# Kernel optimization log

Hardware: AMD Instinct MI355X
Metric: run time of the kernel (lower is better)

Reference implementation:

```python
import jax, jax.numpy as jnp
import numpy as np

W_WIN = 5        # fine_window_size
D_F = 128        # fine d_model
D_C = 256        # coarse d_model
B, HF, WF = 2, 208, 208
WC = 104
LC = WC * WC
N = 5000


def setup_inputs() -> dict:
    key = jax.random.key(0)
    ks = jax.random.split(key, 12)
    inp = {
        'feat_f0': jax.random.normal(ks[0], (B, D_F, HF, WF), jnp.float32),
        'feat_f1': jax.random.normal(ks[1], (B, D_F, HF, WF), jnp.float32),
        'feat_c0': jax.random.normal(ks[2], (B, LC, D_C), jnp.float32),
        'feat_c1': jax.random.normal(ks[3], (B, LC, D_C), jnp.float32),
        # linear layer params (stored as [in, out]; torch weight is [out, in])
        'corr_fuse_w': jax.random.normal(ks[4], (3 * D_F, D_F), jnp.float32) * 0.05,
        'corr_fuse_b': jnp.zeros((D_F,), jnp.float32),
        'down_proj_w': jax.random.normal(ks[5], (D_C, D_F), jnp.float32) * 0.05,
        'down_proj_b': jnp.zeros((D_F,), jnp.float32),
        'merge_feat_w': jax.random.normal(ks[6], (2 * D_F, D_F), jnp.float32) * 0.05,
        'merge_feat_b': jnp.zeros((D_F,), jnp.float32),
        'b_ids': jax.random.randint(ks[7], (N,), 0, B),
        'i_ids': jax.random.randint(ks[8], (N,), 0, LC),
        'j_ids': jax.random.randint(ks[9], (N,), 0, LC),
        'w0c': WC,
        'w1c': WC,
    }
    return inp


def _extract_patches(feat, b_ids, x_ids, y_ids, W):
    # Equivalent to F.unfold(feat, W, stride=1, padding=W//2) followed by a
    # gather at linear index y*width+x: directly gather the WxW window
    # centered at (x, y) with zero padding. feat: [B, C, H, Wd].
    Bsz, C, H, Wd = feat.shape
    off = jnp.arange(W) - W // 2
    yy = (y_ids[:, None] + off)[:, :, None]          # [n, W, 1]
    xx = (x_ids[:, None] + off)[:, None, :]          # [n, 1, W]
    valid = (yy >= 0) & (yy < H) & (xx >= 0) & (xx < Wd)  # [n, W, W]
    yc = jnp.clip(yy, 0, H - 1)
    xc = jnp.clip(xx, 0, Wd - 1)
    # advanced-index gather -> [n, W, W, C] (kernel rows outer, cols inner,
    # channel last: matches unfold's C-major layout after view/transpose)
    p = feat[b_ids[:, None, None], :, yc, xc]
    p = p * valid[..., None].astype(feat.dtype)
    return p.reshape(p.shape[0], W * W, C)           # [n, ww, C]


def reference(feat_f0, feat_f1, feat_c0, feat_c1,
              corr_fuse_w, corr_fuse_b, down_proj_w, down_proj_b,
              merge_feat_w, merge_feat_b,
              b_ids, i_ids, j_ids, w0c, w1c):
    W = W_WIN
    ww = W * W
    d_f = feat_f0.shape[1]
    Hf0, Wf0 = feat_f0.shape[2], feat_f0.shape[3]
    Hf1, Wf1 = feat_f1.shape[2], feat_f1.shape[3]

    x0 = jnp.clip((i_ids % w0c) * 2, 0, Wf0 - 1)
    y0 = jnp.clip((i_ids // w0c) * 2, 0, Hf0 - 1)
    x1 = jnp.clip((j_ids % w1c) * 2, 0, Wf1 - 1)
    y1 = jnp.clip((j_ids // w1c) * 2, 0, Hf1 - 1)

    p0 = _extract_patches(feat_f0, b_ids, x0, y0, W)   # [N, ww, d_f]
    p1 = _extract_patches(feat_f1, b_ids, x1, y1, W)

    inv_s = 1.0 / (d_f ** 0.5)
    c_patch = p0 * p1 * inv_s
    ctx_map = feat_f1.mean(axis=(2, 3))[b_ids][:, None, :]   # [N, 1, d_f]
    c_uav = p0 * ctx_map * inv_s
    ctx_uav = feat_f0.mean(axis=(2, 3))[b_ids][:, None, :]
    c_map = p1 * ctx_uav * inv_s

    f0 = jnp.concatenate([c_patch, c_uav, c_map], -1) @ corr_fuse_w + corr_fuse_b
    f1 = jnp.concatenate([c_patch, c_map, c_uav], -1) @ corr_fuse_w + corr_fuse_b

    # cat_c_feat branch
    fc = jnp.concatenate([feat_c0[b_ids, i_ids], feat_c1[b_ids, j_ids]], 0)
    fc = fc @ down_proj_w + down_proj_b                       # [2N, d_f]
    fc_rep = jnp.broadcast_to(fc[:, None, :], (fc.shape[0], ww, fc.shape[1]))
    merged = jnp.concatenate([jnp.concatenate([f0, f1], 0), fc_rep], -1)
    merged = merged @ merge_feat_w + merge_feat_b             # [2N, ww, d_f]

    n = f0.shape[0]
    return merged[:n], merged[n:]
```

## Files before the change

kernel.cpp:

```cpp
#include <hip/hip_runtime.h>

#define HF   208
#define WF   208
#define D_C  256
#define LC   10816
#define NPTS 5000
#define HW   (HF*WF)
#define INV_S 0.08838834764831845f
#define PAD  136

typedef __bf16 bf16_t;
typedef __bf16 bf16x8 __attribute__((ext_vector_type(8)));
typedef float  f32x4  __attribute__((ext_vector_type(4)));

#define FTR_OFF   172032
#define FTR_BYTES ((size_t)2*2*HW*128*2)
#define G_OFF     (FTR_OFF + FTR_BYTES)
#define G_BYTES   ((size_t)2*NPTS*128*4)

__global__ __launch_bounds__(256) void ptg_kernel(
    const float* __restrict__ f0, const float* __restrict__ f1,
    const float* __restrict__ fc0, const float* __restrict__ fc1,
    const float* __restrict__ corr_w, const float* __restrict__ corr_b,
    const float* __restrict__ dp_w,   const float* __restrict__ dp_b,
    const float* __restrict__ mg_w,   const float* __restrict__ mg_b,
    const int* __restrict__ b_ids, const int* __restrict__ i_ids,
    const int* __restrict__ j_ids,
    bf16_t* __restrict__ A_swz, bf16_t* __restrict__ DmB,
    float* __restrict__ bias_all,
    bf16_t* __restrict__ ftr, float* __restrict__ ctxs,
    float* __restrict__ g) {
  __shared__ union {
    struct { float tile[64][129]; float cred[128]; } tr;
    float s_src[16][256];
  } sm;
  int bid = blockIdx.x;
  int tid = threadIdx.x;

  if (bid < 641) {
    if (tid >= 128) return;
    int c = tid;
    if (bid < 384) {
      int mat = bid >> 7, r = bid & 127;
      float acc = 0.f;
      for (int t = 0; t < 128; ++t)
        acc += corr_w[(mat * 128 + r) * 128 + t] * mg_w[t * 128 + c];
      if (mat == 0) acc *= INV_S;
      int ks = r >> 5, quad = (r & 31) >> 3, jj = r & 7;
      int nt = c >> 4, lr = c & 15;
      A_swz[mat * 16384 + (((nt * 4 + ks) * 64) + quad * 16 + lr) * 8 + jj] = (bf16_t)acc;
    } else if (bid < 640) {
      int r = bid - 384;
      float acc = 0.f;
      for (int t = 0; t < 128; ++t)
        acc += dp_w[r * 128 + t] * mg_w[(128 + t) * 128 + c];
      DmB[(((r >> 3) * 128) + c) * 8 + (r & 7)] = (bf16_t)acc;
    } else {
      float acc = mg_b[c];
      for (int t = 0; t < 128; ++t) {
        acc += corr_b[t] * mg_w[t * 128 + c];
        acc += dp_b[t]   * mg_w[(128 + t) * 128 + c];
      }
      bias_all[c] = acc;
    }
    return;
  }

  if (bid >= 3345) {
    int r0 = (bid - 3345) * 16;
    for (int u = tid; u < 16 * 256; u += 256) {
      int rr = u >> 8, t = u & 255;
      int r = r0 + rr;
      const float* src;
      int b, idx;
      if (r < NPTS) { b = b_ids[r]; idx = i_ids[r]; src = fc0; }
      else          { b = b_ids[r - NPTS]; idx = j_ids[r - NPTS]; src = fc1; }
      sm.s_src[rr][t] = src[((size_t)b * LC + idx) * D_C + t];
    }
    __syncthreads();
    int col = tid & 127, half = tid >> 7;
    float h[8];
    {
      float db = dp_b[col];
#pragma unroll
      for (int r8 = 0; r8 < 8; ++r8) h[r8] = db;
      for (int t = 0; t < 256; t += 4) {
        f32x4 wv;
#pragma unroll
        for (int k = 0; k < 4; ++k) wv[k] = dp_w[(t + k) * 128 + col];
#pragma unroll
        for (int r8 = 0; r8 < 8; ++r8) {
          f32x4 sv = *(const f32x4*)&sm.s_src[half * 8 + r8][t];
          h[r8] += sv[0] * wv[0] + sv[1] * wv[1] + sv[2] * wv[2] + sv[3] * wv[3];
        }
      }
    }
    __syncthreads();
    float* s_h = &sm.s_src[0][0];
#pragma unroll
    for (int r8 = 0; r8 < 8; ++r8) s_h[(half * 8 + r8) * 128 + col] = h[r8];
    __syncthreads();
    float acc2[8];
    float mb = mg_b[col];
#pragma unroll
    for (int r8 = 0; r8 < 8; ++r8) acc2[r8] = mb;
    for (int t = 0; t < 128; t += 4) {
      f32x4 wv;
#pragma unroll
      for (int k = 0; k < 4; ++k) wv[k] = mg_w[(128 + t + k) * 128 + col];
#pragma unroll
      for (int r8 = 0; r8 < 8; ++r8) {
        f32x4 sv = *(const f32x4*)&s_h[(half * 8 + r8) * 128 + t];
        acc2[r8] += sv[0] * wv[0] + sv[1] * wv[1] + sv[2] * wv[2] + sv[3] * wv[3];
      }
    }
    float cp = 0.f;
    for (int t = 0; t < 128; ++t) cp += corr_b[t] * mg_w[t * 128 + col];
#pragma unroll
    for (int r8 = 0; r8 < 8; ++r8)
      g[(size_t)(r0 + half * 8 + r8) * 128 + col] = acc2[r8] + cp;
    return;
  }

  bid -= 641;
  int tb = bid / 676;
  int hw0 = (bid % 676) * 64;
  const float* src = (tb < 2 ? f0 : f1) + (size_t)((tb & 1) * 128) * HW;
  if (tid < 128) sm.tr.cred[tid] = 0.f;
  int w4 = (tid & 15) * 4, cr = tid >> 4;
  for (int c = cr; c < 128; c += 16) {
    f32x4 v = *(const f32x4*)&src[(size_t)c * HW + hw0 + w4];
#pragma unroll
    for (int j = 0; j < 4; ++j) sm.tr.tile[w4 + j][c] = v[j];
  }
  __syncthreads();
  bf16_t* dst = ftr + ((size_t)tb * HW + hw0) * 128;
  int cb = (tid & 15) * 8;
  float sums8[8] = {0, 0, 0, 0, 0, 0, 0, 0};
  for (int p = (tid >> 4); p < 64; p += 16) {
    bf16x8 v;
#pragma unroll
    for (int j = 0; j < 8; ++j) {
      float x = sm.tr.tile[p][cb + j];
      sums8[j] += x;
      v[j] = (bf16_t)x;
    }
    *(bf16x8*)(dst + (size_t)p * 128 + cb) = v;
  }
  int lane = tid & 63;
#pragma unroll
  for (int j = 0; j < 8; ++j) {
    float s = sums8[j];
    s += __shfl_down(s, 32, 64);
    s += __shfl_down(s, 16, 64);
    if (lane < 16) atomicAdd(&sm.tr.cred[cb + j], s);
  }
  __syncthreads();
  if (tid < 128) atomicAdd(&ctxs[tb * 128 + tid], sm.tr.cred[tid]);
}

__global__ __launch_bounds__(256, 6) void main_kernel(
    const bf16_t* __restrict__ ftr,
    const int* __restrict__ b_ids, const int* __restrict__ i_ids,
    const int* __restrict__ j_ids, const int* __restrict__ w0c_p,
    const int* __restrict__ w1c_p, const float* __restrict__ ctxs,
    const bf16_t* __restrict__ A_swz, const float* __restrict__ g,
    float* __restrict__ out) {
  __shared__ __align__(16) union {
    bf16_t sV[3][32][PAD];
    float  so[2][25 * 128];
  } sm;

  int n = blockIdx.x;
  int tid = threadIdx.x;
  int b = b_ids[n], ii = i_ids[n], jj = j_ids[n];
  int w0c = w0c_p[0], w1c = w1c_p[0];
  int x0 = min((ii % w0c) * 2, WF - 1), y0 = min((ii / w0c) * 2, HF - 1);
  int x1 = min((jj % w1c) * 2, WF - 1), y1 = min((jj / w1c) * 2, HF - 1);

  int grp = tid >> 3, e = tid & 7;
  if (grp < 25) {
    const bf16_t* base0 = ftr + (size_t)b * HW * 128;
    const bf16_t* base1 = ftr + (size_t)(2 + b) * HW * 128;
    int dy = grp / 5 - 2, dx = grp % 5 - 2;
    int ya = y0 + dy, xa = x0 + dx;
    int yb = y1 + dy, xb = x1 + dx;
    bool v0 = (ya >= 0 && ya < HF && xa >= 0 && xa < WF);
    bool v1 = (yb >= 0 && yb < HF && xb >= 0 && xb < WF);
    const bf16_t* r0 = base0 + ((size_t)(v0 ? ya * WF + xa : 0)) * 128;
    const bf16_t* r1 = base1 + ((size_t)(v1 ? yb * WF + xb : 0)) * 128;
    const float ksc = INV_S / (float)HW;
#pragma unroll
    for (int h = 0; h < 2; ++h) {
      int cb = h * 64 + e * 8;
      bf16x8 a0 = *(const bf16x8*)(r0 + cb);
      bf16x8 a1 = *(const bf16x8*)(r1 + cb);
      f32x4 cs0a = *(const f32x4*)&ctxs[b * 128 + cb];
      f32x4 cs0b = *(const f32x4*)&ctxs[b * 128 + cb + 4];
      f32x4 cs1a = *(const f32x4*)&ctxs[256 + b * 128 + cb];
      f32x4 cs1b = *(const f32x4*)&ctxs[256 + b * 128 + cb + 4];
      bf16x8 oP, o1, o2;
#pragma unroll
      for (int j = 0; j < 8; ++j) {
        float p0 = v0 ? (float)a0[j] : 0.f;
        float p1 = v1 ? (float)a1[j] : 0.f;
        float c0f = (j < 4 ? cs0a[j & 3] : cs0b[j & 3]) * ksc;
        float c1f = (j < 4 ? cs1a[j & 3] : cs1b[j & 3]) * ksc;
        oP[j] = (bf16_t)(p0 * p1);
        o1[j] = (bf16_t)(p0 * c1f);
        o2[j] = (bf16_t)(p1 * c0f);
      }
      *(bf16x8*)&sm.sV[0][grp][cb] = oP;
      *(bf16x8*)&sm.sV[1][grp][cb] = o1;
      *(bf16x8*)&sm.sV[2][grp][cb] = o2;
    }
  }
  __syncthreads();

  int w = tid >> 6, lane = tid & 63, quad = lane >> 4, lr = lane & 15;
  f32x4 accP[2][2] = {};
  f32x4 acc01[2][2] = {};
  f32x4 acc10[2][2] = {};

#pragma unroll
  for (int ks = 0; ks < 4; ++ks) {
    bf16x8 va[2][3];
#pragma unroll
    for (int mt = 0; mt < 2; ++mt)
#pragma unroll
      for (int m = 0; m < 3; ++m)
        va[mt][m] = *(const bf16x8*)&sm.sV[m][mt * 16 + lr][ks * 32 + quad * 8];
    bf16x8 vb[3][2];
#pragma unroll
    for (int m = 0; m < 3; ++m)
#pragma unroll
      for (int ntl = 0; ntl < 2; ++ntl) {
        int nt = w * 2 + ntl;
        vb[m][ntl] = *(const bf16x8*)(A_swz + m * 16384 + (((nt * 4 + ks) * 64) + lane) * 8);
      }
#pragma unroll
    for (int mt = 0; mt < 2; ++mt)
#pragma unroll
      for (int ntl = 0; ntl < 2; ++ntl) {
        accP[mt][ntl]  = __builtin_amdgcn_mfma_f32_16x16x32_bf16(va[mt][0], vb[0][ntl], accP[mt][ntl], 0, 0, 0);
        acc01[mt][ntl] = __builtin_amdgcn_mfma_f32_16x16x32_bf16(va[mt][1], vb[1][ntl], acc01[mt][ntl], 0, 0, 0);
        acc01[mt][ntl] = __builtin_amdgcn_mfma_f32_16x16x32_bf16(va[mt][2], vb[2][ntl], acc01[mt][ntl], 0, 0, 0);
        acc10[mt][ntl] = __builtin_amdgcn_mfma_f32_16x16x32_bf16(va[mt][2], vb[1][ntl], acc10[mt][ntl], 0, 0, 0);
        acc10[mt][ntl] = __builtin_amdgcn_mfma_f32_16x16x32_bf16(va[mt][1], vb[2][ntl], acc10[mt][ntl], 0, 0, 0);
      }
  }
  __syncthreads();

#pragma unroll
  for (int ntl = 0; ntl < 2; ++ntl) {
    int col = w * 32 + ntl * 16 + lr;
#pragma unroll
    for (int mt = 0; mt < 2; ++mt)
#pragma unroll
      for (int rg = 0; rg < 4; ++rg) {
        int row = mt * 16 + quad * 4 + rg;
        if (row < 25) {
          sm.so[0][row * 128 + col] = accP[mt][ntl][rg] + acc01[mt][ntl][rg];
          sm.so[1][row * 128 + col] = accP[mt][ntl][rg] + acc10[mt][ntl][rg];
        }
      }
  }
  __syncthreads();

  float* o0 = out + (size_t)n * 3200;
  float* o1 = out + (size_t)NPTS * 3200 + (size_t)n * 3200;
  const float* g0 = g + (size_t)n * 128;
  const float* g1 = g + (size_t)(NPTS + n) * 128;
  for (int i = tid; i < 800; i += 256) {
    int f = i * 4, c = f & 127;
    f32x4 gv0 = *(const f32x4*)(g0 + c);
    f32x4 gv1 = *(const f32x4*)(g1 + c);
    f32x4 v0 = *(const f32x4*)&sm.so[0][f];
    f32x4 v1 = *(const f32x4*)&sm.so[1][f];
    __builtin_nontemporal_store(v0 + gv0, (f32x4*)(o0 + f));
    __builtin_nontemporal_store(v1 + gv1, (f32x4*)(o1 + f));
  }
}

__global__ __launch_bounds__(256) void ctx_mean_f32_kernel(
    const float* __restrict__ f0, const float* __restrict__ f1,
    float* __restrict__ ctxs) {
  int id = blockIdx.x;
  const float* src = (id < 256 ? f0 : f1) + (size_t)(id & 255) * HW;
  float s = 0.f;
  for (int i = threadIdx.x; i < HW; i += 256) s += src[i];
  for (int off = 32; off > 0; off >>= 1) s += __shfl_down(s, off, 64);
  __shared__ float part[4];
  if ((threadIdx.x & 63) == 0) part[threadIdx.x >> 6] = s;
  __syncthreads();
  if (threadIdx.x == 0) ctxs[id] = part[0] + part[1] + part[2] + part[3];
}

__global__ __launch_bounds__(256, 4) void main_fallback_kernel(
    const float* __restrict__ f0, const float* __restrict__ f1,
    const float* __restrict__ fc0, const float* __restrict__ fc1,
    const int* __restrict__ b_ids, const int* __restrict__ i_ids,
    const int* __restrict__ j_ids, const int* __restrict__ w0c_p,
    const int* __restrict__ w1c_p, const float* __restrict__ ctxs,
    const float* __restrict__ bias_all, const bf16_t* __restrict__ A_swz,
    const bf16_t* __restrict__ DmB, float* __restrict__ out) {
  __shared__ __align__(16) bf16_t sV[3][32][PAD];
  __shared__ float sg[2][128];
  int n = blockIdx.x;
  int tid = threadIdx.x;
  int b = b_ids[n], ii = i_ids[n], jj = j_ids[n];
  int w0c = w0c_p[0], w1c = w1c_p[0];
  int x0 = min((ii % w0c) * 2, WF - 1), y0 = min((ii / w0c) * 2, HF - 1);
  int x1 = min((jj % w1c) * 2, WF - 1), y1 = min((jj / w1c) * 2, HF - 1);
  const float ksc = INV_S / (float)HW;
  int c = tid & 127, kh = tid >> 7;
  float cs0 = ctxs[b * 128 + c] * ksc;
  float cs1 = ctxs[256 + b * 128 + c] * ksc;
  const float* f0b = f0 + (size_t)(b * 128 + c) * HW;
  const float* f1b = f1 + (size_t)(b * 128 + c) * HW;
  for (int k = kh; k < 32; k += 2) {
    float p0 = 0.f, p1 = 0.f;
    if (k < 25) {
      int dy = k / 5 - 2, dx = k % 5 - 2;
      int ya = y0 + dy, xa = x0 + dx;
      if (ya >= 0 && ya < HF && xa >= 0 && xa < WF) p0 = f0b[ya * WF + xa];
      int yb = y1 + dy, xb = x1 + dx;
      if (yb >= 0 && yb < HF && xb >= 0 && xb < WF) p1 = f1b[yb * WF + xb];
    }
    sV[0][k][c] = (bf16_t)(p0 * p1);
    sV[1][k][c] = (bf16_t)(p0 * cs1);
    sV[2][k][c] = (bf16_t)(p1 * cs0);
  }
  {
    int h = tid >> 7, col = tid & 127;
    const float* fcrow = h ? fc1 + ((size_t)b * LC + jj) * D_C
                           : fc0 + ((size_t)b * LC + ii) * D_C;
    const bf16_t* dbase = DmB + col * 8;
    float p0 = 0.f, p1 = 0.f, p2 = 0.f, p3 = 0.f;
#pragma unroll 4
    for (int t8 = 0; t8 < 32; ++t8) {
      bf16x8 d  = *(const bf16x8*)(dbase + t8 * 1024);
      f32x4  fa = *(const f32x4*)(fcrow + t8 * 8);
      f32x4  fb = *(const f32x4*)(fcrow + t8 * 8 + 4);
      p0 += fa[0] * (float)d[0] + fb[0] * (float)d[4];
      p1 += fa[1] * (float)d[1] + fb[1] * (float)d[5];
      p2 += fa[2] * (float)d[2] + fb[2] * (float)d[6];
      p3 += fa[3] * (float)d[3] + fb[3] * (float)d[7];
    }
    sg[h][col] = ((p0 + p1) + (p2 + p3));
  }
  __syncthreads();
  int w = tid >> 6, lane = tid & 63, quad = lane >> 4, lr = lane & 15;
  f32x4 accP[2][2] = {}, acc01[2][2] = {}, acc10[2][2] = {};
#pragma unroll
  for (int ks = 0; ks < 4; ++ks) {
    bf16x8 va[2][3];
#pragma unroll
    for (int mt = 0; mt < 2; ++mt)
#pragma unroll
      for (int m = 0; m < 3; ++m)
        va[mt][m] = *(const bf16x8*)&sV[m][mt * 16 + lr][ks * 32 + quad * 8];
    bf16x8 vb[3][2];
#pragma unroll
    for (int m = 0; m < 3; ++m)
#pragma unroll
      for (int ntl = 0; ntl < 2; ++ntl) {
        int nt = w * 2 + ntl;
        vb[m][ntl] = *(const bf16x8*)(A_swz + m * 16384 + (((nt * 4 + ks) * 64) + lane) * 8);
      }
#pragma unroll
    for (int mt = 0; mt < 2; ++mt)
#pragma unroll
      for (int ntl = 0; ntl < 2; ++ntl) {
        accP[mt][ntl]  = __builtin_amdgcn_mfma_f32_16x16x32_bf16(va[mt][0], vb[0][ntl], accP[mt][ntl], 0, 0, 0);
        acc01[mt][ntl] = __builtin_amdgcn_mfma_f32_16x16x32_bf16(va[mt][1], vb[1][ntl], acc01[mt][ntl], 0, 0, 0);
        acc01[mt][ntl] = __builtin_amdgcn_mfma_f32_16x16x32_bf16(va[mt][2], vb[2][ntl], acc01[mt][ntl], 0, 0, 0);
        acc10[mt][ntl] = __builtin_amdgcn_mfma_f32_16x16x32_bf16(va[mt][2], vb[1][ntl], acc10[mt][ntl], 0, 0, 0);
        acc10[mt][ntl] = __builtin_amdgcn_mfma_f32_16x16x32_bf16(va[mt][1], vb[2][ntl], acc10[mt][ntl], 0, 0, 0);
      }
  }
#pragma unroll
  for (int ntl = 0; ntl < 2; ++ntl) {
    int col = w * 32 + ntl * 16 + lr;
    float bg = bias_all[col];
    float gg0 = sg[0][col] + bg, gg1 = sg[1][col] + bg;
#pragma unroll
    for (int mt = 0; mt < 2; ++mt)
#pragma unroll
      for (int rg = 0; rg < 4; ++rg) {
        int row = mt * 16 + quad * 4 + rg;
        if (row < 25) {
          size_t o = ((size_t)n * 25 + row) * 128 + col;
          out[o] = accP[mt][ntl][rg] + acc01[mt][ntl][rg] + gg0;
          out[(size_t)NPTS * 25 * 128 + o] = accP[mt][ntl][rg] + acc10[mt][ntl][rg] + gg1;
        }
      }
  }
}

extern "C" void kernel_launch(void* const* d_in, const int* in_sizes, int n_in,
                              void* d_out, int out_size, void* d_ws, size_t ws_size,
                              hipStream_t stream) {
  const float* f0     = (const float*)d_in[0];
  const float* f1     = (const float*)d_in[1];
  const float* fc0    = (const float*)d_in[2];
  const float* fc1    = (const float*)d_in[3];
  const float* corr_w = (const float*)d_in[4];
  const float* corr_b = (const float*)d_in[5];
  const float* dp_w   = (const float*)d_in[6];
  const float* dp_b   = (const float*)d_in[7];
  const float* mg_w   = (const float*)d_in[8];
  const float* mg_b   = (const float*)d_in[9];
  const int* b_ids    = (const int*)d_in[10];
  const int* i_ids    = (const int*)d_in[11];
  const int* j_ids    = (const int*)d_in[12];
  const int* w0c      = (const int*)d_in[13];
  const int* w1c      = (const int*)d_in[14];

  char* ws = (char*)d_ws;
  float*  ctxs     = (float*)(ws);
  float*  bias_all = (float*)(ws + 4096);
  bf16_t* A_swz    = (bf16_t*)(ws + 8192);
  bf16_t* DmB      = (bf16_t*)(ws + 106496);
  bf16_t* ftr      = (bf16_t*)(ws + FTR_OFF);
  float*  g        = (float*)(ws + G_OFF);
  int fast = (ws_size >= G_OFF + G_BYTES) ? 1 : 0;

  if (fast) {
    hipMemsetAsync(ctxs, 0, 2048, stream);
    ptg_kernel<<<3970, 256, 0, stream>>>(
        f0, f1, fc0, fc1, corr_w, corr_b, dp_w, dp_b, mg_w, mg_b,
        b_ids, i_ids, j_ids, A_swz, DmB, bias_all, ftr, ctxs, g);
    main_kernel<<<NPTS, 256, 0, stream>>>(ftr, b_ids, i_ids, j_ids, w0c, w1c,
                                          ctxs, A_swz, g, (float*)d_out);
  } else {
    ptg_kernel<<<641, 256, 0, stream>>>(
        f0, f1, fc0, fc1, corr_w, corr_b, dp_w, dp_b, mg_w, mg_b,
        b_ids, i_ids, j_ids, A_swz, DmB, bias_all, ftr, ctxs, g);
    ctx_mean_f32_kernel<<<512, 256, 0, stream>>>(f0, f1, ctxs);
    main_fallback_kernel<<<NPTS, 256, 0, stream>>>(f0, f1, fc0, fc1, b_ids,
                                                   i_ids, j_ids, w0c, w1c, ctxs,
                                                   bias_all, A_swz, DmB,
                                                   (float*)d_out);
  }
}
```

Before: 347.7 us.

## Store transpose tile as bf16, reduce channel sums in registers, reorder block roles

The transpose part of the prep kernel now converts to bf16 when writing the shared-memory tile, which halves LDS use. It computes per-channel sums with 16-lane shuffles straight from the loaded vectors, so the second pass over shared memory and the shared atomics go away, and it writes rows with vector bf16x8 reads. The g-projection blocks are moved to the front of the grid and the launch bounds ask for 8 blocks per CU, so the heavier work starts early and occupancy rises. The fallback path has to detect its smaller grid by checking gridDim, which adds coupling between the two paths.

```diff
diff --git a/kernel.cpp b/kernel.cpp
--- a/kernel.cpp
+++ b/kernel.cpp
@@ -9,6 +9,11 @@
 #define INV_S 0.08838834764831845f
 #define PAD  136
 
+#define G_BLOCKS    625
+#define PREP_BLOCKS 641
+#define TR_BLOCKS   2704
+#define PTG_GRID    (G_BLOCKS + PREP_BLOCKS + TR_BLOCKS)
+
 typedef __bf16 bf16_t;
 typedef __bf16 bf16x8 __attribute__((ext_vector_type(8)));
 typedef float  f32x4  __attribute__((ext_vector_type(4)));
@@ -18,7 +23,7 @@
 #define G_OFF     (FTR_OFF + FTR_BYTES)
 #define G_BYTES   ((size_t)2*NPTS*128*4)
 
-__global__ __launch_bounds__(256) void ptg_kernel(
+__global__ __launch_bounds__(256, 8) void ptg_kernel(
     const float* __restrict__ f0, const float* __restrict__ f1,
     const float* __restrict__ fc0, const float* __restrict__ fc1,
     const float* __restrict__ corr_w, const float* __restrict__ corr_b,
@@ -30,18 +35,25 @@
     float* __restrict__ bias_all,
     bf16_t* __restrict__ ftr, float* __restrict__ ctxs,
     float* __restrict__ g) {
-  __shared__ union {
-    struct { float tile[64][129]; float cred[128]; } tr;
+  __shared__ __align__(16) union {
+    struct { bf16_t tile[64][136]; float cred[128]; } tr;
     float s_src[16][256];
   } sm;
   int bid = blockIdx.x;
   int tid = threadIdx.x;
 
-  if (bid < 641) {
+  int prep_id = -1;
+  if (gridDim.x == 641) {
+    prep_id = bid;
+  } else if (bid >= G_BLOCKS && bid < G_BLOCKS + PREP_BLOCKS) {
+    prep_id = bid - G_BLOCKS;
+  }
+
+  if (prep_id >= 0) {
     if (tid >= 128) return;
     int c = tid;
-    if (bid < 384) {
-      int mat = bid >> 7, r = bid & 127;
+    if (prep_id < 384) {
+      int mat = prep_id >> 7, r = prep_id & 127;
       float acc = 0.f;
       for (int t = 0; t < 128; ++t)
         acc += corr_w[(mat * 128 + r) * 128 + t] * mg_w[t * 128 + c];
@@ -49,8 +61,8 @@
       int ks = r >> 5, quad = (r & 31) >> 3, jj = r & 7;
       int nt = c >> 4, lr = c & 15;
       A_swz[mat * 16384 + (((nt * 4 + ks) * 64) + quad * 16 + lr) * 8 + jj] = (bf16_t)acc;
-    } else if (bid < 640) {
-      int r = bid - 384;
+    } else if (prep_id < 640) {
+      int r = prep_id - 384;
       float acc = 0.f;
       for (int t = 0; t < 128; ++t)
         acc += dp_w[r * 128 + t] * mg_w[(128 + t) * 128 + c];
@@ -66,8 +78,8 @@
     return;
   }
 
-  if (bid >= 3345) {
-    int r0 = (bid - 3345) * 16;
+  if (bid < G_BLOCKS) {
+    int r0 = bid * 16;
     for (int u = tid; u < 16 * 256; u += 256) {
       int rr = u >> 8, t = u & 255;
       int r = r0 + rr;
@@ -122,41 +134,40 @@
     return;
   }
 
-  bid -= 641;
-  int tb = bid / 676;
-  int hw0 = (bid % 676) * 64;
+  int tbid = bid - (G_BLOCKS + PREP_BLOCKS);
+  int tb = tbid / 676;
+  int hw0 = (tbid % 676) * 64;
   const float* src = (tb < 2 ? f0 : f1) + (size_t)((tb & 1) * 128) * HW;
-  if (tid < 128) sm.tr.cred[tid] = 0.f;
-  int w4 = (tid & 15) * 4, cr = tid >> 4;
-  for (int c = cr; c < 128; c += 16) {
+  int wg = tid & 15, cr = tid >> 4;
+  int w4 = wg * 4;
+  float csum[8];
+#pragma unroll
+  for (int k = 0; k < 8; ++k) {
+    int c = cr + k * 16;
     f32x4 v = *(const f32x4*)&src[(size_t)c * HW + hw0 + w4];
-#pragma unroll
-    for (int j = 0; j < 4; ++j) sm.tr.tile[w4 + j][c] = v[j];
-  }
-  __syncthreads();
+    csum[k] = (v[0] + v[1]) + (v[2] + v[3]);
+#pragma unroll
+    for (int j = 0; j < 4; ++j) sm.tr.tile[w4 + j][c] = (bf16_t)v[j];
+  }
+#pragma unroll
+  for (int k = 0; k < 8; ++k) {
+    float s = csum[k];
+    s += __shfl_down(s, 8, 16);
+    s += __shfl_down(s, 4, 16);
+    s += __shfl_down(s, 2, 16);
+    s += __shfl_down(s, 1, 16);
+    if (wg == 0) sm.tr.cred[cr + k * 16] = s;
+  }
+  __syncthreads();
+  if (tid < 128) atomicAdd(&ctxs[tb * 128 + tid], sm.tr.cred[tid]);
   bf16_t* dst = ftr + ((size_t)tb * HW + hw0) * 128;
-  int cb = (tid & 15) * 8;
-  float sums8[8] = {0, 0, 0, 0, 0, 0, 0, 0};
-  for (int p = (tid >> 4); p < 64; p += 16) {
-    bf16x8 v;
-#pragma unroll
-    for (int j = 0; j < 8; ++j) {
-      float x = sm.tr.tile[p][cb + j];
-      sums8[j] += x;
-      v[j] = (bf16_t)x;
-    }
+  int cb = wg * 8;
+#pragma unroll
+  for (int i = 0; i < 4; ++i) {
+    int p = cr + 16 * i;
+    bf16x8 v = *(const bf16x8*)&sm.tr.tile[p][cb];
     *(bf16x8*)(dst + (size_t)p * 128 + cb) = v;
   }
-  int lane = tid & 63;
-#pragma unroll
-  for (int j = 0; j < 8; ++j) {
-    float s = sums8[j];
-    s += __shfl_down(s, 32, 64);
-    s += __shfl_down(s, 16, 64);
-    if (lane < 16) atomicAdd(&sm.tr.cred[cb + j], s);
-  }
-  __syncthreads();
-  if (tid < 128) atomicAdd(&ctxs[tb * 128 + tid], sm.tr.cred[tid]);
 }
 
 __global__ __launch_bounds__(256, 6) void main_kernel(
@@ -428,7 +439,7 @@
 
   if (fast) {
     hipMemsetAsync(ctxs, 0, 2048, stream);
-    ptg_kernel<<<3970, 256, 0, stream>>>(
+    ptg_kernel<<<PTG_GRID, 256, 0, stream>>>(
         f0, f1, fc0, fc1, corr_w, corr_b, dp_w, dp_b, mg_w, mg_b,
         b_ids, i_ids, j_ids, A_swz, DmB, bias_all, ftr, ctxs, g);
     main_kernel<<<NPTS, 256, 0, stream>>>(ftr, b_ids, i_ids, j_ids, w0c, w1c,
```

After: 330.0 us. 5.1% less time.
